# Kernel tuning notes

Hardware: AMD Instinct MI355X
Metric: run time of the kernel (lower is better)

Reference implementation:

```python
import jax, jax.numpy as jnp
import numpy as np

B, S, D, H, DQ, DK = 2, 2048, 1024, 16, 64, 64


def setup_inputs() -> dict:
    key = jax.random.key(0)
    ks = jax.random.split(key, 11)
    s = 0.02
    return {
        "query": jax.random.normal(ks[0], (B, S, D), jnp.float32),
        "key": jax.random.normal(ks[1], (B, S, D), jnp.float32),
        "value": jax.random.normal(ks[2], (B, S, D), jnp.float32),
        "Wq": jax.random.normal(ks[3], (H, D, DQ), jnp.float32) * s,
        "bq": jax.random.normal(ks[4], (H, DQ), jnp.float32) * s,
        "Wk": jax.random.normal(ks[5], (H, D, DK), jnp.float32) * s,
        "bk": jax.random.normal(ks[6], (H, DK), jnp.float32) * s,
        "Wv": jax.random.normal(ks[7], (H, D, DK), jnp.float32) * s,
        "bv": jax.random.normal(ks[8], (H, DK), jnp.float32) * s,
        "Wo": jax.random.normal(ks[9], (H * DK, D), jnp.float32) * s,
        "bo": jax.random.normal(ks[10], (D,), jnp.float32) * s,
    }


def reference(query, key, value, Wq, bq, Wk, bk, Wv, bv, Wo, bo):
    # Per-head linear projections (batched over heads): [B,H,S,dq/dk]
    q = jnp.einsum('bsd,hde->bhse', query, Wq) + bq[None, :, None, :]
    k = jnp.einsum('bsd,hde->bhse', key, Wk) + bk[None, :, None, :]
    v = jnp.einsum('bsd,hde->bhse', value, Wv) + bv[None, :, None, :]
    # Scaled dot-product attention: softmax(QK^T / sqrt(dim_q)) V
    scale = 1.0 / jnp.sqrt(jnp.asarray(q.shape[-1], q.dtype))
    scores = jnp.einsum('bhse,bhte->bhst', q, k) * scale  # [B,H,S,S]
    attn = jax.nn.softmax(scores, axis=-1)
    out = jnp.einsum('bhst,bhte->bhse', attn, v)  # [B,H,S,dk]
    # Concat heads along feature dim, then output linear
    cat = out.transpose(0, 2, 1, 3).reshape(out.shape[0], out.shape[2], -1)  # [B,S,H*dk]
    return cat @ Wo + bo
```

## Files before the change

kernel.cpp:

```cpp
#include <hip/hip_runtime.h>
#include <hip/hip_bf16.h>
#include <math.h>

#define NB 2
#define NS 2048
#define ND 1024
#define NH 16
#define DH 64
#define MROWS (NB*NS)
#define NCOLS (NH*DH)

typedef __attribute__((ext_vector_type(8))) short bf16x8;
typedef __attribute__((ext_vector_type(4))) float f32x4;
typedef __attribute__((ext_vector_type(16))) float f32x16;
typedef __attribute__((ext_vector_type(8))) unsigned short ushort8t;
typedef unsigned short ushort;

extern "C" __device__ float __ocml_native_exp2_f32(float);
#define EXP2F(x) __ocml_native_exp2_f32(x)
#define LOG2E 1.44269504088896f

static __device__ __forceinline__ ushort f2bf(float f) {
    union { __hip_bfloat16 b; ushort u; } cv;
    cv.b = __hip_bfloat16(f);
    return cv.u;
}

static __device__ __forceinline__ unsigned cvtpk(float a, float b) {
    unsigned r;
    asm("v_cvt_pk_bf16_f32 %0, %1, %2" : "=v"(r) : "v"(a), "v"(b));
    return r;
}

static __device__ __forceinline__ float fmax3(float a, float b, float c) {
    return fmaxf(fmaxf(a, b), c);
}

static __device__ __forceinline__ void gld_lds16(const void* g, void* l) {
    __builtin_amdgcn_global_load_lds(
        (const __attribute__((address_space(1))) void*)g,
        (__attribute__((address_space(3))) void*)l, 16, 0, 0);
}

__global__ __launch_bounds__(256) void prep_kernel(
    const float* __restrict__ q, const float* __restrict__ k,
    const float* __restrict__ v, ushort* __restrict__ X_bf,
    const float* __restrict__ Wq, const float* __restrict__ Wk,
    const float* __restrict__ Wv, ushort* __restrict__ WT_bf,
    const float* __restrict__ Wo, ushort* __restrict__ WoT_bf)
{
    const int bx = blockIdx.x;
    const int t = threadIdx.x;
    __shared__ float tile[64][65];

    if (bx < 2048) {
        const size_t n1 = (size_t)MROWS * ND;
        const size_t off = ((size_t)bx * 256 + t) * 8;
        const float* srcs[3] = {q, k, v};
        #pragma unroll
        for (int p = 0; p < 3; ++p) {
            float4 a = *(const float4*)(srcs[p] + off);
            float4 b = *(const float4*)(srcs[p] + off + 4);
            ushort8t w;
            w[0]=f2bf(a.x); w[1]=f2bf(a.y); w[2]=f2bf(a.z); w[3]=f2bf(a.w);
            w[4]=f2bf(b.x); w[5]=f2bf(b.y); w[6]=f2bf(b.z); w[7]=f2bf(b.w);
            *(ushort8t*)(X_bf + (size_t)p * n1 + off) = w;
        }
    } else if (bx < 2816) {
        const int i2 = bx - 2048;
        const int p = i2 >> 8;
        const int r = i2 & 255;
        const int h = r >> 4, d0 = (r & 15) * 64;
        const float* W = (p == 0) ? Wq : (p == 1) ? Wk : Wv;
        {
            const int i = t >> 2, e0 = (t & 3) * 16;
            const float* src = W + ((size_t)h * ND + d0 + i) * DH + e0;
            #pragma unroll
            for (int u = 0; u < 4; ++u) {
                float4 v4 = ((const float4*)src)[u];
                tile[i][e0 + u*4 + 0] = v4.x; tile[i][e0 + u*4 + 1] = v4.y;
                tile[i][e0 + u*4 + 2] = v4.z; tile[i][e0 + u*4 + 3] = v4.w;
            }
        }
        __syncthreads();
        {
            const int e = t >> 2, dc = (t & 3) * 16;
            ushort* dst = WT_bf + ((size_t)p * NCOLS + h * 64 + e) * ND + d0 + dc;
            ushort8t w0, w1;
            #pragma unroll
            for (int u = 0; u < 8; ++u) { w0[u] = f2bf(tile[dc+u][e]); w1[u] = f2bf(tile[dc+8+u][e]); }
            *(ushort8t*)dst = w0;
            *(ushort8t*)(dst + 8) = w1;
        }
    } else {
        const int i3 = bx - 2816;
        const int f0 = (i3 & 15) * 64, c0 = (i3 >> 4) * 64;
        {
            const int i = t >> 2, j0 = (t & 3) * 16;
            const float* src = Wo + (size_t)(f0 + i) * ND + c0 + j0;
            #pragma unroll
            for (int u = 0; u < 4; ++u) {
                float4 v4 = ((const float4*)src)[u];
                tile[i][j0 + u*4 + 0] = v4.x; tile[i][j0 + u*4 + 1] = v4.y;
                tile[i][j0 + u*4 + 2] = v4.z; tile[i][j0 + u*4 + 3] = v4.w;
            }
        }
        __syncthreads();
        {
            const int cl = t >> 2, fc = (t & 3) * 16;
            ushort* dst = WoT_bf + (size_t)(c0 + cl) * ND + f0 + fc;
            ushort8t w0, w1;
            #pragma unroll
            for (int u = 0; u < 8; ++u) { w0[u] = f2bf(tile[fc+u][cl]); w1[u] = f2bf(tile[fc+8+u][cl]); }
            *(ushort8t*)dst = w0;
            *(ushort8t*)(dst + 8) = w1;
        }
    }
}

__global__ __launch_bounds__(256) void gemm_qkv(
    const ushort* __restrict__ X_bf, const ushort* __restrict__ WT_bf,
    const float* __restrict__ bq, const float* __restrict__ bk,
    const float* __restrict__ bv, ushort* __restrict__ qkv_bf,
    ushort* __restrict__ vT_bf)
{
    const int p = blockIdx.z;
    const float* bias = (p == 0) ? bq : (p == 1) ? bk : bv;
    const float scale = (p == 0) ? 0.125f * LOG2E : 1.0f;
    const int m0 = blockIdx.x * 128, n0 = blockIdx.y * 128;
    const int t = threadIdx.x, wid = t >> 6, lane = t & 63;
    const int wr = wid >> 1, wc = wid & 1;
    const int c = lane & 15, g = lane >> 4;

    __shared__ ushort ldsAB[2 * 128 * 64];
    ushort* ldsA = ldsAB;
    ushort* ldsB = ldsAB + 128 * 64;

    const ushort* Ag = X_bf + (size_t)p * MROWS * ND + (size_t)m0 * ND;
    const ushort* Bg = WT_bf + (size_t)p * NCOLS * ND + (size_t)n0 * ND;

    f32x4 acc[4][4];
    #pragma unroll
    for (int m = 0; m < 4; ++m)
        #pragma unroll
        for (int n = 0; n < 4; ++n)
            acc[m][n] = (f32x4){0.f, 0.f, 0.f, 0.f};

    for (int k0 = 0; k0 < ND; k0 += 64) {
        __syncthreads();
        #pragma unroll
        for (int call = 0; call < 4; ++call) {
            const int ch = wid * 256 + call * 64 + lane;
            const int row = ch >> 3, c16 = ch & 7;
            gld_lds16(Ag + (size_t)row * ND + k0 + c16 * 8, ldsA + (size_t)ch * 8);
            gld_lds16(Bg + (size_t)row * ND + k0 + c16 * 8, ldsB + (size_t)ch * 8);
        }
        __syncthreads();
        #pragma unroll
        for (int kc = 0; kc < 2; ++kc) {
            bf16x8 af[4], bfr[4];
            #pragma unroll
            for (int m = 0; m < 4; ++m)
                af[m] = *(const bf16x8*)(ldsA + (wr*64 + m*16 + c) * 64 + kc*32 + g*8);
            #pragma unroll
            for (int n = 0; n < 4; ++n)
                bfr[n] = *(const bf16x8*)(ldsB + (wc*64 + n*16 + c) * 64 + kc*32 + g*8);
            #pragma unroll
            for (int m = 0; m < 4; ++m)
                #pragma unroll
                for (int n = 0; n < 4; ++n)
                    acc[m][n] = __builtin_amdgcn_mfma_f32_16x16x32_bf16(af[m], bfr[n], acc[m][n], 0, 0, 0);
        }
    }

    if (p == 2) {
        #pragma unroll
        for (int m = 0; m < 4; ++m) {
            const int s0b = m0 + wr*64 + m*16 + g*4;
            const int b = s0b >> 11, sl = s0b & (NS - 1);
            #pragma unroll
            for (int n = 0; n < 4; ++n) {
                const int gc = n0 + wc*64 + n*16 + c;
                const int h = gc >> 6, e = gc & 63;
                const float bv_ = bias[gc];
                uint2 wv;
                wv.x = cvtpk(acc[m][n][0] + bv_, acc[m][n][1] + bv_);
                wv.y = cvtpk(acc[m][n][2] + bv_, acc[m][n][3] + bv_);
                *(uint2*)(vT_bf + ((size_t)(b * NH + h) * DH + e) * NS + sl) = wv;
            }
        }
    } else {
        __syncthreads();
        ushort* ldsC = ldsAB;
        #pragma unroll
        for (int m = 0; m < 4; ++m)
            #pragma unroll
            for (int n = 0; n < 4; ++n) {
                const int col = wc*64 + n*16 + c;
                const float bv_ = bias[n0 + col];
                #pragma unroll
                for (int j = 0; j < 4; ++j) {
                    const int row = wr*64 + m*16 + g*4 + j;
                    ldsC[row * 128 + col] = f2bf((acc[m][n][j] + bv_) * scale);
                }
            }
        __syncthreads();
        ushort* dstbase = qkv_bf + (size_t)p * ((size_t)NB * NH * NS * DH);
        #pragma unroll
        for (int rr = 0; rr < 8; ++rr) {
            const int idx = rr * 256 + t;
            const int row = idx >> 4;
            const int col0 = (idx & 15) * 8;
            const int gc = n0 + col0;
            const int h = gc >> 6, e0 = gc & 63;
            const int gr = m0 + row;
            const int b = gr >> 11, s = gr & (NS - 1);
            ushort8t w = *(ushort8t*)(ldsC + row * 128 + col0);
            *(ushort8t*)(dstbase + (((size_t)b * NH + h) * NS + s) * DH + e0) = w;
        }
    }
}

__global__ __launch_bounds__(256) void attn_kernel(
    const ushort* __restrict__ q_bf, const ushort* __restrict__ k_bf,
    const ushort* __restrict__ vT_bf, ushort* __restrict__ cat_bf)
{
    __shared__ __attribute__((aligned(16))) char smem[32768];
    const int t = threadIdx.x;
    const int wid = t >> 6, lane = t & 63;
    const int ql = lane & 31;
    const int hi = lane >> 5;

    const int linear = blockIdx.x;
    const int xcd = linear & 7;
    const int idx = linear >> 3;
    const int bh = xcd * 4 + (idx >> 4);
    const int qx = idx & 15;
    const int qrow0 = qx * 128 + wid * 32;

    bf16x8 qf[4];
    {
        const char* qp = (const char*)(q_bf + ((size_t)bh * NS + qrow0 + ql) * DH);
        #pragma unroll
        for (int ds = 0; ds < 4; ++ds)
            qf[ds] = *(const bf16x8*)(qp + ds * 32 + hi * 16);
    }

    f32x16 o_acc[2];
    #pragma unroll
    for (int et = 0; et < 2; ++et)
        #pragma unroll
        for (int i = 0; i < 16; ++i)
            o_acc[et][i] = 0.f;
    float m = -INFINITY, lsum = 0.f;

    const char* kg = (const char*)(k_bf + (size_t)bh * NS * DH);
    const char* vg = (const char*)(vT_bf + (size_t)bh * DH * NS);

    const int ch0 = t * 2;
    const int row0 = ch0 >> 3, c16a = ch0 & 7;
    const int c16b = c16a + 1;
    const int swz0 = (c16a * 16) ^ ((row0 & 7) << 4);
    const int swz1 = (c16b * 16) ^ ((row0 & 7) << 4);

    ushort8t kr0, kr1, vr0, vr1;

    #define ATTN_LOAD(JT) do { \
        kr0 = *(const ushort8t*)(kg + (size_t)((JT) + row0) * 128 + c16a * 16); \
        kr1 = *(const ushort8t*)(kg + (size_t)((JT) + row0) * 128 + c16b * 16); \
        vr0 = *(const ushort8t*)(vg + (size_t)row0 * (NS*2) + (size_t)((JT) + c16a*8) * 2); \
        vr1 = *(const ushort8t*)(vg + (size_t)row0 * (NS*2) + (size_t)((JT) + c16b*8) * 2); \
    } while (0)

    #define ATTN_STORE(BUF) do { \
        char* Kd = smem + (BUF) * 8192; \
        char* Vd = smem + 16384 + (BUF) * 8192; \
        *(ushort8t*)(Kd + row0 * 128 + swz0) = kr0; \
        *(ushort8t*)(Kd + row0 * 128 + swz1) = kr1; \
        *(ushort8t*)(Vd + row0 * 128 + swz0) = vr0; \
        *(ushort8t*)(Vd + row0 * 128 + swz1) = vr1; \
    } while (0)

    ATTN_LOAD(0);
    ATTN_STORE(0);
    __syncthreads();
    int cur = 0;

    for (int jt = 0; jt < NS; jt += 64) {
        ATTN_LOAD((jt + 64) & (NS - 1));

        const char* Ks  = smem + cur * 8192;
        const char* VTs = smem + 16384 + cur * 8192;

        f32x16 s_acc[2];
        #pragma unroll
        for (int kt = 0; kt < 2; ++kt)
            #pragma unroll
            for (int i = 0; i < 16; ++i)
                s_acc[kt][i] = 0.f;
        __builtin_amdgcn_s_setprio(1);
        #pragma unroll
        for (int ds = 0; ds < 4; ++ds) {
            #pragma unroll
            for (int kt = 0; kt < 2; ++kt) {
                const int key = kt * 32 + ql;
                bf16x8 kf = *(const bf16x8*)(Ks + key * 128 + ((ds*32 + hi*16) ^ ((key & 7) << 4)));
                s_acc[kt] = __builtin_amdgcn_mfma_f32_32x32x16_bf16(kf, qf[ds], s_acc[kt], 0, 0, 0);
            }
        }
        __builtin_amdgcn_s_setprio(0);

        float tm = fmaxf(s_acc[0][0], s_acc[0][1]);
        #pragma unroll
        for (int i = 2; i < 16; i += 2) tm = fmax3(tm, s_acc[0][i], s_acc[0][i+1]);
        #pragma unroll
        for (int i = 0; i < 16; i += 2) tm = fmax3(tm, s_acc[1][i], s_acc[1][i+1]);
        if (!__all(tm <= m + 11.5f)) {
            const float tm2 = fmaxf(tm, __shfl_xor(tm, 32));
            const float mnew = fmaxf(m, tm2);
            const float sc = EXP2F(m - mnew);
            lsum *= sc;
            #pragma unroll
            for (int et = 0; et < 2; ++et)
                #pragma unroll
                for (int i = 0; i < 16; ++i)
                    o_acc[et][i] *= sc;
            m = mnew;
        }

        float rs = 0.f;
        #pragma unroll
        for (int kt = 0; kt < 2; ++kt) {
            float pe[16];
            #pragma unroll
            for (int i = 0; i < 16; ++i) {
                pe[i] = EXP2F(s_acc[kt][i] - m);
                rs += pe[i];
            }
            unsigned a0 = cvtpk(pe[0],  pe[1]);
            unsigned a1 = cvtpk(pe[2],  pe[3]);
            unsigned b0 = cvtpk(pe[4],  pe[5]);
            unsigned b1 = cvtpk(pe[6],  pe[7]);
            asm volatile("v_permlane32_swap_b32 %0, %1" : "+v"(a0), "+v"(b0));
            asm volatile("v_permlane32_swap_b32 %0, %1" : "+v"(a1), "+v"(b1));
            unsigned c0 = cvtpk(pe[8],  pe[9]);
            unsigned c1 = cvtpk(pe[10], pe[11]);
            unsigned d0 = cvtpk(pe[12], pe[13]);
            unsigned d1 = cvtpk(pe[14], pe[15]);
            asm volatile("v_permlane32_swap_b32 %0, %1" : "+v"(c0), "+v"(d0));
            asm volatile("v_permlane32_swap_b32 %0, %1" : "+v"(c1), "+v"(d1));
            union { bf16x8 v; unsigned u[4]; } B0, B1;
            B0.u[0] = a0; B0.u[1] = a1; B0.u[2] = b0; B0.u[3] = b1;
            B1.u[0] = c0; B1.u[1] = c1; B1.u[2] = d0; B1.u[3] = d1;

            __builtin_amdgcn_s_setprio(1);
            #pragma unroll
            for (int et = 0; et < 2; ++et) {
                const int e = et * 32 + ql;
                bf16x8 vf0 = *(const bf16x8*)(VTs + e * 128 + (((2*kt)   * 32 + hi*16) ^ ((e & 7) << 4)));
                o_acc[et] = __builtin_amdgcn_mfma_f32_32x32x16_bf16(vf0, B0.v, o_acc[et], 0, 0, 0);
                bf16x8 vf1 = *(const bf16x8*)(VTs + e * 128 + (((2*kt+1) * 32 + hi*16) ^ ((e & 7) << 4)));
                o_acc[et] = __builtin_amdgcn_mfma_f32_32x32x16_bf16(vf1, B1.v, o_acc[et], 0, 0, 0);
            }
            __builtin_amdgcn_s_setprio(0);
        }
        lsum += rs;

        ATTN_STORE(cur ^ 1);
        __syncthreads();
        cur ^= 1;
    }

    lsum += __shfl_xor(lsum, 32);
    const float inv = 1.0f / lsum;

    const int b = bh >> 4, hh = bh & 15;
    const int s = qrow0 + ql;
    ushort* op = cat_bf + ((size_t)b * NS + s) * NCOLS + hh * DH;
    #pragma unroll
    for (int et = 0; et < 2; ++et) {
        #pragma unroll
        for (int rgrp = 0; rgrp < 4; ++rgrp) {
            uint2 wv;
            wv.x = cvtpk(o_acc[et][rgrp*4+0] * inv, o_acc[et][rgrp*4+1] * inv);
            wv.y = cvtpk(o_acc[et][rgrp*4+2] * inv, o_acc[et][rgrp*4+3] * inv);
            *(uint2*)(op + et*32 + rgrp*8 + hi*4) = wv;
        }
    }
    #undef ATTN_LOAD
    #undef ATTN_STORE
}

__global__ __launch_bounds__(256) void gemm_out(
    const ushort* __restrict__ cat_bf, const ushort* __restrict__ WoT_bf,
    const float* __restrict__ bo, float* __restrict__ out)
{
    const int m0 = blockIdx.x * 128, n0 = blockIdx.y * 128;
    const int t = threadIdx.x, wid = t >> 6, lane = t & 63;
    const int wr = wid >> 1, wc = wid & 1;
    const int c = lane & 15, g = lane >> 4;

    __shared__ ushort ldsA[128 * 64];
    __shared__ ushort ldsB[128 * 64];

    const ushort* Ag = cat_bf + (size_t)m0 * ND;
    const ushort* Bg = WoT_bf + (size_t)n0 * ND;

    f32x4 acc[4][4];
    #pragma unroll
    for (int m = 0; m < 4; ++m)
        #pragma unroll
        for (int n = 0; n < 4; ++n)
            acc[m][n] = (f32x4){0.f, 0.f, 0.f, 0.f};

    for (int k0 = 0; k0 < ND; k0 += 64) {
        __syncthreads();
        #pragma unroll
        for (int call = 0; call < 4; ++call) {
            const int ch = wid * 256 + call * 64 + lane;
            const int row = ch >> 3, c16 = ch & 7;
            gld_lds16(Ag + (size_t)row * ND + k0 + c16 * 8, ldsA + (size_t)ch * 8);
            gld_lds16(Bg + (size_t)row * ND + k0 + c16 * 8, ldsB + (size_t)ch * 8);
        }
        __syncthreads();
        #pragma unroll
        for (int kc = 0; kc < 2; ++kc) {
            bf16x8 af[4], bfr[4];
            #pragma unroll
            for (int m = 0; m < 4; ++m)
                af[m] = *(const bf16x8*)(ldsA + (wr*64 + m*16 + c) * 64 + kc*32 + g*8);
            #pragma unroll
            for (int n = 0; n < 4; ++n)
                bfr[n] = *(const bf16x8*)(ldsB + (wc*64 + n*16 + c) * 64 + kc*32 + g*8);
            #pragma unroll
            for (int m = 0; m < 4; ++m)
                #pragma unroll
                for (int n = 0; n < 4; ++n)
                    acc[m][n] = __builtin_amdgcn_mfma_f32_16x16x32_bf16(af[m], bfr[n], acc[m][n], 0, 0, 0);
        }
    }

    #pragma unroll
    for (int m = 0; m < 4; ++m) {
        const int gr0 = m0 + wr*64 + m*16 + g*4;
        #pragma unroll
        for (int n = 0; n < 4; ++n) {
            const int gc = n0 + wc*64 + n*16 + c;
            const float bv_ = bo[gc];
            #pragma unroll
            for (int j = 0; j < 4; ++j)
                out[(size_t)(gr0 + j) * ND + gc] = acc[m][n][j] + bv_;
        }
    }
}

extern "C" void kernel_launch(void* const* d_in, const int* in_sizes, int n_in,
                              void* d_out, int out_size, void* d_ws, size_t ws_size,
                              hipStream_t stream) {
    const float* query = (const float*)d_in[0];
    const float* key_  = (const float*)d_in[1];
    const float* value = (const float*)d_in[2];
    const float* Wq = (const float*)d_in[3];
    const float* bq = (const float*)d_in[4];
    const float* Wk = (const float*)d_in[5];
    const float* bk = (const float*)d_in[6];
    const float* Wv = (const float*)d_in[7];
    const float* bv = (const float*)d_in[8];
    const float* Wo = (const float*)d_in[9];
    const float* bo = (const float*)d_in[10];
    float* out = (float*)d_out;

    const size_t per = (size_t)NB * NH * NS * DH;
    const size_t xsz = (size_t)MROWS * ND;

    ushort* X_bf   = (ushort*)d_ws;
    ushort* qkv_bf = X_bf + 3 * xsz;
    ushort* vT_bf  = qkv_bf + 3 * per;
    ushort* WT_bf  = vT_bf + per;
    ushort* WoT_bf = WT_bf + (size_t)3 * ND * NCOLS;
    ushort* cat_bf = X_bf;

    prep_kernel<<<3072, 256, 0, stream>>>(query, key_, value, X_bf,
                                          Wq, Wk, Wv, WT_bf, Wo, WoT_bf);

    gemm_qkv<<<dim3(32, 8, 3), 256, 0, stream>>>(X_bf, WT_bf, bq, bk, bv, qkv_bf, vT_bf);

    attn_kernel<<<512, 256, 0, stream>>>(qkv_bf, qkv_bf + per, vT_bf, cat_bf);

    gemm_out<<<dim3(32, 8), 256, 0, stream>>>(cat_bf, WoT_bf, bo, out);
}
```

Baseline: 238.5 us.

## Split attention over key halves with a separate merge kernel

Each attention block now processes only half of the key sequence, which doubles the grid from 512 to 1024 blocks. Each block writes a partial normalized output in bf16 plus its running max and sum. A new merge kernel combines the two halves using log-sum-exp weights and writes the concatenated-head layout consumed by the output GEMM. The aim is better occupancy across the GPU's CUs. The cost is an extra kernel launch, extra global traffic for the partials, and an added bf16 rounding step on the partial outputs.

```diff
diff --git a/kernel.cpp b/kernel.cpp
--- a/kernel.cpp
+++ b/kernel.cpp
@@ -24,6 +24,12 @@
     union { __hip_bfloat16 b; ushort u; } cv;
     cv.b = __hip_bfloat16(f);
     return cv.u;
+}
+
+static __device__ __forceinline__ float bf2f(ushort u) {
+    union { unsigned u; float f; } cv;
+    cv.u = ((unsigned)u) << 16;
+    return cv.f;
 }
 
 static __device__ __forceinline__ unsigned cvtpk(float a, float b) {
@@ -223,7 +229,8 @@
 
 __global__ __launch_bounds__(256) void attn_kernel(
     const ushort* __restrict__ q_bf, const ushort* __restrict__ k_bf,
-    const ushort* __restrict__ vT_bf, ushort* __restrict__ cat_bf)
+    const ushort* __restrict__ vT_bf, ushort* __restrict__ po,
+    float2* __restrict__ pml)
 {
     __shared__ __attribute__((aligned(16))) char smem[32768];
     const int t = threadIdx.x;
@@ -234,9 +241,12 @@
     const int linear = blockIdx.x;
     const int xcd = linear & 7;
     const int idx = linear >> 3;
-    const int bh = xcd * 4 + (idx >> 4);
-    const int qx = idx & 15;
+    const int bh = xcd * 4 + (idx >> 5);
+    const int sub = idx & 31;
+    const int qx = sub >> 1;
+    const int half = sub & 1;
     const int qrow0 = qx * 128 + wid * 32;
+    const int hb = half * 1024;
 
     bf16x8 qf[4];
     {
@@ -281,13 +291,13 @@
         *(ushort8t*)(Vd + row0 * 128 + swz1) = vr1; \
     } while (0)
 
-    ATTN_LOAD(0);
+    ATTN_LOAD(hb);
     ATTN_STORE(0);
     __syncthreads();
     int cur = 0;
 
-    for (int jt = 0; jt < NS; jt += 64) {
-        ATTN_LOAD((jt + 64) & (NS - 1));
+    for (int jt = hb; jt < hb + 1024; jt += 64) {
+        ATTN_LOAD(hb + ((jt - hb + 64) & 1023));
 
         const char* Ks  = smem + cur * 8192;
         const char* VTs = smem + 16384 + cur * 8192;
@@ -374,9 +384,9 @@
     lsum += __shfl_xor(lsum, 32);
     const float inv = 1.0f / lsum;
 
-    const int b = bh >> 4, hh = bh & 15;
     const int s = qrow0 + ql;
-    ushort* op = cat_bf + ((size_t)b * NS + s) * NCOLS + hh * DH;
+    const size_t prow = (size_t)(half * 32 + bh) * NS + s;
+    ushort* op = po + prow * DH;
     #pragma unroll
     for (int et = 0; et < 2; ++et) {
         #pragma unroll
@@ -387,8 +397,44 @@
             *(uint2*)(op + et*32 + rgrp*8 + hi*4) = wv;
         }
     }
+    if (hi == 0) pml[prow] = make_float2(m, lsum);
     #undef ATTN_LOAD
     #undef ATTN_STORE
+}
+
+__global__ __launch_bounds__(256) void merge_kernel(
+    const ushort* __restrict__ po, const float2* __restrict__ pml,
+    ushort* __restrict__ cat_bf)
+{
+    const int row = blockIdx.x * 256 + threadIdx.x;
+    const int bh = row >> 11, s = row & (NS - 1);
+    const int b = bh >> 4, h = bh & 15;
+
+    const float2 ml1 = pml[row];
+    const float2 ml2 = pml[(size_t)32 * NS + row];
+    const float M = fmaxf(ml1.x, ml2.x);
+    const float w1 = ml1.y * EXP2F(ml1.x - M);
+    const float w2 = ml2.y * EXP2F(ml2.x - M);
+    const float inv = 1.0f / (w1 + w2);
+    const float a1 = w1 * inv, a2 = w2 * inv;
+
+    const ushort* p1 = po + (size_t)row * DH;
+    const ushort* p2 = po + ((size_t)32 * NS + row) * DH;
+    ushort* dst = cat_bf + ((size_t)b * NS + s) * NCOLS + h * DH;
+
+    #pragma unroll
+    for (int u = 0; u < 8; ++u) {
+        ushort8t r1 = *(const ushort8t*)(p1 + u * 8);
+        ushort8t r2 = *(const ushort8t*)(p2 + u * 8);
+        union { ushort8t v; unsigned u32[4]; } w;
+        #pragma unroll
+        for (int j = 0; j < 4; ++j) {
+            const float lo = a1 * bf2f(r1[2*j])   + a2 * bf2f(r2[2*j]);
+            const float hh2 = a1 * bf2f(r1[2*j+1]) + a2 * bf2f(r2[2*j+1]);
+            w.u32[j] = cvtpk(lo, hh2);
+        }
+        *(ushort8t*)(dst + u * 8) = w.v;
+    }
 }
 
 __global__ __launch_bounds__(256) void gemm_out(
@@ -479,13 +525,17 @@
     ushort* WT_bf  = vT_bf + per;
     ushort* WoT_bf = WT_bf + (size_t)3 * ND * NCOLS;
     ushort* cat_bf = X_bf;
+    ushort* po     = X_bf + per;
+    float2* pml    = (float2*)(qkv_bf + 2 * per);
 
     prep_kernel<<<3072, 256, 0, stream>>>(query, key_, value, X_bf,
                                           Wq, Wk, Wv, WT_bf, Wo, WoT_bf);
 
     gemm_qkv<<<dim3(32, 8, 3), 256, 0, stream>>>(X_bf, WT_bf, bq, bk, bv, qkv_bf, vT_bf);
 
-    attn_kernel<<<512, 256, 0, stream>>>(qkv_bf, qkv_bf + per, vT_bf, cat_bf);
+    attn_kernel<<<1024, 256, 0, stream>>>(qkv_bf, qkv_bf + per, vT_bf, po, pml);
+
+    merge_kernel<<<256, 256, 0, stream>>>(po, pml, cat_bf);
 
     gemm_out<<<dim3(32, 8), 256, 0, stream>>>(cat_bf, WoT_bf, bo, out);
 }
```

Measured after the change: 252.2 us. +5.7%, slower.
